# Optimization experiments

Hardware: AMD Instinct MI355X
Metric: run time of the kernel (lower is better)

The kernel has to match this reference:

```python
import jax, jax.numpy as jnp
import numpy as np
from jax import lax

# MinkowskiEngine semantics reproduced on a dense grid:
# - a sparse tensor's active set = voxels where any feature channel is nonzero
# - stride-1 conv: output coords == input coords  -> mask output with input mask
# - stride-2 conv (k=5, pad=2): output coords = unique(floor(c/2))  -> 2x2x2 max-pool of mask
# - GlobalPooling: mean of features over active output coords, per batch
# MinkowskiConvolution has no bias by default; MinkowskiLinear has one.

DN = ('NCDHW', 'OIDHW', 'NCDHW')

def conv3d(x, w, stride, pad):
    return lax.conv_general_dilated(
        x, w, (stride, stride, stride), [(pad, pad)] * 3, dimension_numbers=DN)

def pool_mask(m):
    # occupancy of stride-2 output coords: any active voxel in each 2x2x2 block
    B, T, H, W = m.shape
    return m.reshape(B, T // 2, 2, H // 2, 2, W // 2, 2).max(axis=(2, 4, 6))

def setup_inputs() -> dict:
    key = jax.random.key(0)
    ks = jax.random.split(key, 7)
    B, T, C, H, W = 16, 128, 2, 34, 34
    vals = jax.random.normal(ks[0], (B, T, C, H, W), jnp.float32)
    keep = jax.random.bernoulli(ks[1], 0.05, (B, T, 1, H, W)).astype(jnp.float32)
    x = vals * keep
    w1 = jax.random.normal(ks[2], (32, 2, 5, 5, 5), jnp.float32) * 0.05
    w2 = jax.random.normal(ks[3], (64, 32, 5, 5, 5), jnp.float32) * 0.05
    w3 = jax.random.normal(ks[4], (128, 64, 3, 3, 3), jnp.float32) * 0.05
    wl = jax.random.normal(ks[5], (10, 128), jnp.float32) * 0.05
    bl = jnp.zeros((10,), jnp.float32)
    return {"x": x, "w1": w1, "w2": w2, "w3": w3, "wl": wl, "bl": bl}

def reference(x, w1, w2, w3, wl, bl):
    # x: [B, T, C, H, W] -> permute(0,2,1,3,4) -> [B, C, T, H, W]
    dense = jnp.transpose(x, (0, 2, 1, 3, 4))
    # active coordinate set of ME.to_sparse(dense)
    mask = (jnp.abs(dense).sum(axis=1) > 0).astype(dense.dtype)  # [B, T, H, W]
    mask = lax.stop_gradient(mask)
    m1 = mask[:, None]
    h = conv3d(dense, w1, 1, 2) * m1                         # k5 s1, out coords = in coords
    mask2 = pool_mask(mask)                                  # stride-2 output occupancy
    m2 = mask2[:, None]
    h = jax.nn.relu(conv3d(h, w2, 2, 2)) * m2                # k5 s2 + ReLU
    h = jax.nn.relu(conv3d(h, w3, 1, 1)) * m2                # k3 s1 + ReLU
    cnt = jnp.maximum(mask2.sum(axis=(1, 2, 3)), 1.0)[:, None]
    pooled = h.sum(axis=(2, 3, 4)) / cnt                     # global avg over active coords -> [B,128]
    logits = pooled @ wl.T + bl                              # MinkowskiLinear(128,10)
    return jax.nn.softmax(jax.nn.relu(logits), axis=-1)      # ReLU -> Softmax -> ToFeature [B,10]
```

## Files before the change

kernel.cpp:

```cpp
#include <hip/hip_runtime.h>

#define BB 16
#define TT 128
#define HH 34
#define WW 34
#define HWSZ (HH*WW)
#define NP1 (BB*TT*HH*WW)
#define TD 64
#define HD 17
#define WD 17
#define NP2 (BB*TD*HD*WD)
#define NW1 (NP1/64)
#define NW2 (NP2/64)
#define CAP1 262144
#define CAP2 131072
#define G2 1024
#define G3 512

typedef __attribute__((ext_vector_type(8))) short bf16x8;
typedef __attribute__((ext_vector_type(4))) float f32x4;

__device__ inline unsigned short f2bf(float f) {
  unsigned u = __float_as_uint(f);
  unsigned r = (u + 0x7fff + ((u >> 16) & 1)) >> 16;
  return (unsigned short)r;
}
__device__ inline float bf2f(unsigned short s) {
  return __uint_as_float((unsigned)s << 16);
}

__global__ void k_ballot1(const float* __restrict__ x, unsigned long long* __restrict__ b1) {
  int i = blockIdx.x * 256 + threadIdx.x;
  int hw = i % HWSZ;
  int bt = i / HWSZ;
  const float* px = x + (size_t)bt * 2 * HWSZ + hw;
  bool act = (fabsf(px[0]) + fabsf(px[HWSZ])) > 0.0f;
  unsigned long long m = __ballot(act);
  if ((threadIdx.x & 63) == 0) b1[i >> 6] = m;
}

__global__ void k_ballot2(const unsigned long long* __restrict__ b1,
                          unsigned long long* __restrict__ b2) {
  int i = blockIdx.x * 256 + threadIdx.x;
  if (i >= NP2) return;
  int ow = i % WD; int r = i / WD;
  int oh = r % HD; r /= HD;
  int od = r % TD; int b = r / TD;
  bool act = false;
  for (int dt = 0; dt < 2; dt++)
    for (int dh = 0; dh < 2; dh++)
      for (int dw = 0; dw < 2; dw++) {
        int t = od * 2 + dt, h = oh * 2 + dh, w = ow * 2 + dw;
        int lin = ((b * TT + t) * HH + h) * WW + w;
        if ((b1[lin >> 6] >> (lin & 63)) & 1ull) act = true;
      }
  unsigned long long m = __ballot(act);
  if ((threadIdx.x & 63) == 0) b2[i >> 6] = m;
}

__global__ __launch_bounds__(1024) void k_scan(
    const unsigned long long* __restrict__ b1, const unsigned long long* __restrict__ b2,
    int* __restrict__ wb1, int* __restrict__ wb2,
    int* __restrict__ counter1, int* __restrict__ counter2, float* __restrict__ cnt) {
  __shared__ int wsum[16];
  __shared__ int wpre[16];
  __shared__ int tots[2];
  int tid = threadIdx.x, lane = tid & 63, wv = tid >> 6;

  const int CH1 = (NW1 + 1023) / 1024;
  int lo = tid * CH1, hi = min(lo + CH1, NW1);
  int s = 0;
  for (int i = lo; i < hi; i++) s += __popcll(b1[i]);
  int sc = s;
  #pragma unroll
  for (int d = 1; d < 64; d <<= 1) { int y = __shfl_up(sc, d); if (lane >= d) sc += y; }
  if (lane == 63) wsum[wv] = sc;
  __syncthreads();
  if (wv == 0 && lane < 16) {
    int v = wsum[lane];
    int p = v;
    #pragma unroll
    for (int d = 1; d < 16; d <<= 1) { int y = __shfl_up(p, d); if (lane >= d) p += y; }
    wpre[lane] = p - v;
    if (lane == 15) tots[0] = p;
  }
  __syncthreads();
  {
    int base = wpre[wv] + (sc - s);
    for (int i = lo; i < hi; i++) { wb1[i] = base; base += __popcll(b1[i]); }
  }
  if (tid == 0) *counter1 = tots[0];
  __syncthreads();

  const int CH2 = (NW2 + 1023) / 1024;
  lo = tid * CH2; hi = min(lo + CH2, NW2);
  s = 0;
  for (int i = lo; i < hi; i++) s += __popcll(b2[i]);
  sc = s;
  #pragma unroll
  for (int d = 1; d < 64; d <<= 1) { int y = __shfl_up(sc, d); if (lane >= d) sc += y; }
  if (lane == 63) wsum[wv] = sc;
  __syncthreads();
  if (wv == 0 && lane < 16) {
    int v = wsum[lane];
    int p = v;
    #pragma unroll
    for (int d = 1; d < 16; d <<= 1) { int y = __shfl_up(p, d); if (lane >= d) p += y; }
    wpre[lane] = p - v;
    if (lane == 15) tots[1] = p;
  }
  __syncthreads();
  {
    int base = wpre[wv] + (sc - s);
    for (int i = lo; i < hi; i++) { wb2[i] = base; base += __popcll(b2[i]); }
  }
  if (tid == 0) *counter2 = tots[1];
  __syncthreads();
  if (tid < 16) {
    int c0 = wb2[tid * 289];
    int c1 = (tid == 15) ? tots[1] : wb2[(tid + 1) * 289];
    cnt[tid] = (float)(c1 - c0);
  }
}

__global__ void k_fill1(const unsigned long long* __restrict__ b1,
                        const int* __restrict__ wb1, int* __restrict__ idx1) {
  int i = blockIdx.x * 256 + threadIdx.x;
  unsigned long long m = b1[i >> 6];
  int lane = i & 63;
  int p = -1;
  if ((m >> lane) & 1ull) {
    p = wb1[i >> 6] + __popcll(m & ((1ull << lane) - 1ull));
    if (p >= CAP1) p = -1;
  }
  idx1[i] = p;
}

__global__ void k_fill2(const unsigned long long* __restrict__ b2,
                        const int* __restrict__ wb2,
                        int* __restrict__ idx2, int* __restrict__ list2) {
  int i = blockIdx.x * 256 + threadIdx.x;
  if (i >= NP2) return;
  unsigned long long m = b2[i >> 6];
  int lane = i & 63;
  int p = -1;
  if ((m >> lane) & 1ull) {
    p = wb2[i >> 6] + __popcll(m & ((1ull << lane) - 1ull));
    if (p < CAP2) list2[p] = i; else p = -1;
  }
  idx2[i] = p;
}

__global__ __launch_bounds__(256) void k_conv1e(
    const float* __restrict__ x, const float* __restrict__ w1,
    const unsigned long long* __restrict__ b1, const int* __restrict__ wb1,
    unsigned short* __restrict__ h1c) {
  __shared__ unsigned short w1s[8000];
  __shared__ unsigned int plist[384];
  __shared__ unsigned long long q[4][128];
  __shared__ int pcnt;
  int tid = threadIdx.x;
  int b = blockIdx.x >> 7;
  int t0 = blockIdx.x & 127;
  if (tid == 0) pcnt = 0;
  for (int j = tid; j < 8000; j += 256) w1s[j] = f2bf(w1[j]);
  __syncthreads();
  int slabbase = (b * TT + t0) * HWSZ;
  for (int hw = tid; hw < HWSZ; hw += 256) {
    int lin = slabbase + hw;
    unsigned long long m = b1[lin >> 6];
    int ln = lin & 63;
    if ((m >> ln) & 1ull) {
      int p = wb1[lin >> 6] + __popcll(m & ((1ull << ln) - 1ull));
      if (p < CAP1) {
        int s = atomicAdd(&pcnt, 1);
        if (s < 384) plist[s] = ((unsigned)p << 11) | (unsigned)hw;
      }
    }
  }
  __syncthreads();
  int n = min(pcnt, 384);
  int lane = tid & 63, wid = tid >> 6;
  int oc = lane & 31, c = lane >> 5;
  int woff = (oc * 2 + c) * 125;
  int csh = c * 16;
  int kt = lane / 5, kh = lane - kt * 5;
  const float* xb = x + (size_t)b * TT * 2 * HWSZ;
  for (int li = wid; li < n; li += 4) {
    unsigned e = plist[li];
    int hw = e & 0x7ff;
    int p = e >> 11;
    int h_ = hw / 34, w_ = hw - h_ * 34;
    int cntA = 0;
    unsigned m5 = 0;
    int t2 = 0, h2 = 0;
    if (lane < 25) {
      t2 = t0 + kt - 2;
      h2 = h_ + kh - 2;
      if ((unsigned)t2 < TT && (unsigned)h2 < HH) {
        int kwmin = (w_ < 2) ? (2 - w_) : 0;
        int kwmax = (w_ > 31) ? (35 - w_) : 4;
        int lin = ((b * TT + t2) * HH + h2) * WW + (w_ + kwmin - 2);
        int wi = lin >> 6, sh = lin & 63;
        unsigned long long v = b1[wi] >> sh;
        if (sh > 59) v |= b1[wi + 1] << (64 - sh);
        m5 = ((unsigned)v & ((1u << (kwmax - kwmin + 1)) - 1u)) << kwmin;
        cntA = __popc(m5);
      }
    }
    int inc = cntA;
    #pragma unroll
    for (int d = 1; d < 64; d <<= 1) { int y = __shfl_up(inc, d); if (lane >= d) inc += y; }
    int off = inc - cntA;
    int ne = __shfl(inc, 63);
    unsigned mm = m5;
    while (mm) {
      int kw = __ffs(mm) - 1; mm &= mm - 1;
      int w2 = w_ + kw - 2;
      int xoff = (t2 * 2) * HWSZ + h2 * 34 + w2;
      unsigned short xv0 = f2bf(xb[xoff]);
      unsigned short xv1 = f2bf(xb[xoff + HWSZ]);
      int tap = (kt * 5 + kh) * 5 + kw;
      q[wid][off++] = (unsigned long long)((unsigned)xv0 | ((unsigned)xv1 << 16)) |
                      ((unsigned long long)tap << 32);
    }
    float acc = 0.f;
    for (int e2 = 0; e2 < ne; e2++) {
      unsigned long long ent = q[wid][e2];
      int tap = (int)(ent >> 32);
      float xv = bf2f((unsigned short)((ent >> csh) & 0xffffull));
      acc += xv * bf2f(w1s[woff + tap]);
    }
    float other = __shfl_down(acc, 32);
    if (lane < 32) h1c[(size_t)p * 32 + oc] = f2bf(acc + other);
  }
}

__global__ void k_tw2b(const float* __restrict__ w2, unsigned short* __restrict__ w2b) {
  int i = blockIdx.x * blockDim.x + threadIdx.x;
  if (i >= 125 * 64 * 32) return;
  int c = i & 31; int r = i >> 5;
  int oc = r & 63; int tap = r >> 6;
  w2b[i] = f2bf(w2[((size_t)oc * 32 + c) * 125 + tap]);
}
__global__ void k_tw3b(const float* __restrict__ w3, unsigned short* __restrict__ w3b) {
  int i = blockIdx.x * blockDim.x + threadIdx.x;
  if (i >= 27 * 128 * 64) return;
  int c = i & 63; int r = i >> 6;
  int oc = r & 127; int tap = r >> 7;
  w3b[i] = f2bf(w3[((size_t)oc * 64 + c) * 27 + tap]);
}

#define S2 40
#define M2 128
__global__ __launch_bounds__(256) void k_conv2m(
    const unsigned short* __restrict__ h1c,
    const unsigned short* __restrict__ w2b,
    const int* __restrict__ idx1,
    const int* __restrict__ list2, const int* __restrict__ counter2,
    unsigned short* __restrict__ h2c) {
  __shared__ __align__(16) unsigned short As[2][M2 * S2];
  __shared__ __align__(16) unsigned short Bs[2][64 * S2];
  __shared__ int4 mc[M2];
  __shared__ int klut[125];
  int tid = threadIdx.x;
  int lane = tid & 63, wid = tid >> 6;
  int fr = lane & 15, fq = lane >> 4;
  int wr = wid * 32;
  if (tid < 125) {
    int kt = tid / 25, r2 = tid - kt * 25;
    klut[tid] = kt | ((r2 / 5) << 4) | ((r2 % 5) << 8);
  }
  int count2 = min(*counter2, CAP2);
  int nchunk = (count2 + M2 - 1) >> 7;
  int aspos = tid >> 1, asq = tid & 1;
  int bspos = tid >> 2, bsq = tid & 3;
  int chid = (blockIdx.x & 7) * (G2 >> 3) + (blockIdx.x >> 3);
  __syncthreads();
  for (int ch = chid; ch < nchunk; ch += gridDim.x) {
    __syncthreads();
    if (tid < M2) {
      int p = ch * M2 + tid;
      int m = (p < count2) ? list2[p] : -1;
      int4 qq; qq.x = -1; qq.y = 0; qq.z = 0; qq.w = 0;
      if (m >= 0) {
        int ow = m % WD; int r = m / WD;
        int oh = r % HD; r /= HD;
        qq.x = r / TD; qq.y = r % TD; qq.z = oh; qq.w = ow;
      }
      mc[tid] = qq;
    }
    __syncthreads();
    int4 q = mc[aspos];
    int tb = q.y * 2 - 2, hb = q.z * 2 - 2, wbv = q.w * 2 - 2;
    bool bok = q.x >= 0;
    auto rowfor = [&](int tap) -> int {
      int k = klut[tap];
      int t = tb + (k & 15), h = hb + ((k >> 4) & 15), w = wbv + (k >> 8);
      int row = -1;
      if (bok && (unsigned)t < TT && (unsigned)h < HH && (unsigned)w < WW)
        row = idx1[((q.x * TT + t) * HH + h) * WW + w];
      return row;
    };
    f32x4 acc[2][4];
    #pragma unroll
    for (int i = 0; i < 2; i++)
      #pragma unroll
      for (int j = 0; j < 4; j++) acc[i][j] = (f32x4){0.f, 0.f, 0.f, 0.f};
    int rowN1;
    int4 rA0 = {0,0,0,0}, rA1 = {0,0,0,0}, rB;
    {
      int r0 = rowfor(0);
      if (r0 >= 0) {
        const unsigned short* s = h1c + (size_t)r0 * 32 + asq * 16;
        rA0 = *(const int4*)s;
        rA1 = *(const int4*)(s + 8);
      }
      rB = *(const int4*)(w2b + (size_t)bspos * 32 + bsq * 8);
      rowN1 = rowfor(1);
    }
    for (int tap = 0; tap < 125; ++tap) {
      int bsel = tap & 1;
      {
        unsigned short* ad = &As[bsel][aspos * S2 + asq * 16];
        *(int4*)(ad) = rA0;
        *(int4*)(ad + 8) = rA1;
        *(int4*)(&Bs[bsel][bspos * S2 + bsq * 8]) = rB;
      }
      bool more = tap < 124;
      if (more) {
        int4 v0 = {0,0,0,0}, v1 = {0,0,0,0};
        if (rowN1 >= 0) {
          const unsigned short* s = h1c + (size_t)rowN1 * 32 + asq * 16;
          v0 = *(const int4*)s;
          v1 = *(const int4*)(s + 8);
        }
        rA0 = v0; rA1 = v1;
        rB = *(const int4*)(w2b + (size_t)(tap + 1) * 2048 + bspos * 32 + bsq * 8);
        rowN1 = (tap < 123) ? rowfor(tap + 2) : -1;
      }
      __syncthreads();
      const unsigned short* ap = &As[bsel][(wr + fr) * S2 + fq * 8];
      const unsigned short* bp = &Bs[bsel][fr * S2 + fq * 8];
      bf16x8 a0 = *(const bf16x8*)ap;
      bf16x8 a1 = *(const bf16x8*)(ap + 16 * S2);
      #pragma unroll
      for (int ni = 0; ni < 4; ni++) {
        bf16x8 bfrag = *(const bf16x8*)(bp + ni * 16 * S2);
        acc[0][ni] = __builtin_amdgcn_mfma_f32_16x16x32_bf16(a0, bfrag, acc[0][ni], 0, 0, 0);
        acc[1][ni] = __builtin_amdgcn_mfma_f32_16x16x32_bf16(a1, bfrag, acc[1][ni], 0, 0, 0);
      }
    }
    int base = ch * M2;
    #pragma unroll
    for (int mi = 0; mi < 2; mi++)
      #pragma unroll
      for (int ni = 0; ni < 4; ni++)
        #pragma unroll
        for (int j = 0; j < 4; j++) {
          int r = wr + mi * 16 + fq * 4 + j;
          int p = base + r;
          if (p < count2) {
            int col = ni * 16 + fr;
            h2c[(size_t)p * 64 + col] = f2bf(fmaxf(acc[mi][ni][j], 0.f));
          }
        }
  }
}

#define S3 72
#define SH3 132
__global__ __launch_bounds__(256) void k_conv3m(
    const unsigned short* __restrict__ h2c,
    const unsigned short* __restrict__ w3b,
    const int* __restrict__ idx2,
    const int* __restrict__ list2, const int* __restrict__ counter2,
    float* __restrict__ partial) {
  __shared__ __align__(16) unsigned short As[2][64 * S3];
  __shared__ __align__(16) unsigned short Bs[2][128 * S3];
  __shared__ float pools[2048];
  __shared__ int rowsL[27 * 64];
  __shared__ int4 mc[64];
  __shared__ int posb[64];
  int tid = threadIdx.x;
  int lane = tid & 63, wid = tid >> 6;
  int fr = lane & 15, fq = lane >> 4;
  int wr = (wid >> 1) * 32, wc = (wid & 1) * 64;
  for (int j = tid; j < 2048; j += 256) pools[j] = 0.f;
  int count2 = min(*counter2, CAP2);
  int nchunk = (count2 + 63) >> 6;
  int spos = tid >> 2, sq = tid & 3;
  int boc = tid >> 1, bh = tid & 1;
  int chid = (blockIdx.x & 7) * (G3 >> 3) + (blockIdx.x >> 3);
  for (int ch = chid; ch < nchunk; ch += gridDim.x) {
    __syncthreads();
    if (tid < 64) {
      int p = ch * 64 + tid;
      int m = (p < count2) ? list2[p] : -1;
      int4 q; q.x = -1; q.y = 0; q.z = 0; q.w = 0;
      if (m >= 0) {
        int ow = m % WD; int r = m / WD;
        int oh = r % HD; r /= HD;
        q.x = r / TD; q.y = r % TD; q.z = oh; q.w = ow;
      }
      mc[tid] = q;
      posb[tid] = (q.x >= 0) ? q.x : 0;
    }
    __syncthreads();
    for (int j = tid; j < 27 * 64; j += 256) {
      int tap = j >> 6, pos = j & 63;
      int4 q = mc[pos];
      int row = -1;
      if (q.x >= 0) {
        int dt = tap / 9 - 1, dh = (tap / 3) % 3 - 1, dw = tap % 3 - 1;
        int t = q.y + dt, h = q.z + dh, w = q.w + dw;
        if ((unsigned)t < TD && (unsigned)h < HD && (unsigned)w < WD)
          row = idx2[((q.x * TD + t) * HD + h) * WD + w];
      }
      rowsL[j] = row;
    }
    __syncthreads();
    f32x4 acc[2][4];
    #pragma unroll
    for (int i = 0; i < 2; i++)
      #pragma unroll
      for (int j = 0; j < 4; j++) acc[i][j] = (f32x4){0.f, 0.f, 0.f, 0.f};
    int4 rA0 = {0, 0, 0, 0}, rA1 = {0, 0, 0, 0};
    {
      int row = rowsL[spos];
      if (row >= 0) {
        const unsigned short* s = h2c + (size_t)row * 64 + sq * 16;
        rA0 = *(const int4*)s;
        rA1 = *(const int4*)(s + 8);
      }
    }
    int4 rB0, rB1, rB2, rB3;
    {
      const unsigned short* wsrc = w3b + (size_t)boc * 64 + bh * 32;
      rB0 = *(const int4*)(wsrc);
      rB1 = *(const int4*)(wsrc + 8);
      rB2 = *(const int4*)(wsrc + 16);
      rB3 = *(const int4*)(wsrc + 24);
    }
    for (int tap = 0; tap < 27; tap++) {
      int bsel = tap & 1;
      {
        unsigned short* ad = &As[bsel][spos * S3 + sq * 16];
        *(int4*)(ad) = rA0;
        *(int4*)(ad + 8) = rA1;
        unsigned short* bd = &Bs[bsel][boc * S3 + bh * 32];
        *(int4*)(bd) = rB0;
        *(int4*)(bd + 8) = rB1;
        *(int4*)(bd + 16) = rB2;
        *(int4*)(bd + 24) = rB3;
      }
      if (tap < 26) {
        int row = rowsL[(tap + 1) * 64 + spos];
        int4 v0 = {0, 0, 0, 0}, v1 = {0, 0, 0, 0};
        if (row >= 0) {
          const unsigned short* s = h2c + (size_t)row * 64 + sq * 16;
          v0 = *(const int4*)s;
          v1 = *(const int4*)(s + 8);
        }
        rA0 = v0; rA1 = v1;
        const unsigned short* wsrc = w3b + ((size_t)(tap + 1) * 128 + boc) * 64 + bh * 32;
        rB0 = *(const int4*)(wsrc);
        rB1 = *(const int4*)(wsrc + 8);
        rB2 = *(const int4*)(wsrc + 16);
        rB3 = *(const int4*)(wsrc + 24);
      }
      __syncthreads();
      const unsigned short* ap = &As[bsel][(wr + fr) * S3 + fq * 8];
      const unsigned short* bp = &Bs[bsel][(wc + fr) * S3 + fq * 8];
      #pragma unroll
      for (int kk = 0; kk < 2; kk++) {
        bf16x8 a0 = *(const bf16x8*)(ap + kk * 32);
        bf16x8 a1 = *(const bf16x8*)(ap + 16 * S3 + kk * 32);
        #pragma unroll
        for (int ni = 0; ni < 4; ni++) {
          bf16x8 bfrag = *(const bf16x8*)(bp + ni * 16 * S3 + kk * 32);
          acc[0][ni] = __builtin_amdgcn_mfma_f32_16x16x32_bf16(a0, bfrag, acc[0][ni], 0, 0, 0);
          acc[1][ni] = __builtin_amdgcn_mfma_f32_16x16x32_bf16(a1, bfrag, acc[1][ni], 0, 0, 0);
        }
      }
    }
    __syncthreads();
    unsigned short* h3 = &As[0][0];
    #pragma unroll
    for (int mi = 0; mi < 2; mi++)
      #pragma unroll
      for (int ni = 0; ni < 4; ni++)
        #pragma unroll
        for (int j = 0; j < 4; j++) {
          int r = wr + mi * 16 + fq * 4 + j;
          int col = wc + ni * 16 + fr;
          h3[r * SH3 + col] = f2bf(fmaxf(acc[mi][ni][j], 0.f));
        }
    __syncthreads();
    if (tid < 128) {
      for (int r = 0; r < 64; r++)
        pools[posb[r] * 128 + tid] += bf2f(h3[r * SH3 + tid]);
    }
  }
  __syncthreads();
  for (int j = tid; j < 2048; j += 256)
    partial[(size_t)blockIdx.x * 2048 + j] = pools[j];
}

__global__ __launch_bounds__(256) void k_red(
    const float* __restrict__ partial, float* __restrict__ pooled) {
  __shared__ float red[256];
  int o = blockIdx.x * 16 + (threadIdx.x & 15);
  int sl = threadIdx.x >> 4;
  float s = 0.f;
  for (int g = sl; g < G3; g += 16) s += partial[(size_t)g * 2048 + o];
  red[threadIdx.x] = s;
  __syncthreads();
  if (threadIdx.x < 16) {
    float t = 0.f;
    #pragma unroll
    for (int k = 0; k < 16; k++) t += red[k * 16 + threadIdx.x];
    pooled[o] = t;
  }
}

__global__ void k_fin(const float* __restrict__ pooled, const float* __restrict__ cnt,
                      const float* __restrict__ wl, const float* __restrict__ bl,
                      float* __restrict__ out) {
  __shared__ float pr[128];
  __shared__ float lg[10];
  int b = blockIdx.x;
  int tid = threadIdx.x;
  pr[tid] = pooled[b * 128 + tid] / fmaxf(cnt[b], 1.0f);
  __syncthreads();
  if (tid < 10) {
    float acc = bl[tid];
    for (int j = 0; j < 128; j++) acc += pr[j] * wl[tid * 128 + j];
    lg[tid] = fmaxf(acc, 0.f);
  }
  __syncthreads();
  if (tid == 0) {
    float mx = lg[0];
    for (int k = 1; k < 10; k++) mx = fmaxf(mx, lg[k]);
    float se = 0.f;
    for (int k = 0; k < 10; k++) se += expf(lg[k] - mx);
    for (int k = 0; k < 10; k++) out[b * 10 + k] = expf(lg[k] - mx) / se;
  }
}

extern "C" void kernel_launch(void* const* d_in, const int* in_sizes, int n_in,
                              void* d_out, int out_size, void* d_ws, size_t ws_size,
                              hipStream_t stream) {
  const float* x  = (const float*)d_in[0];
  const float* w1 = (const float*)d_in[1];
  const float* w2 = (const float*)d_in[2];
  const float* w3 = (const float*)d_in[3];
  const float* wl = (const float*)d_in[4];
  const float* bl = (const float*)d_in[5];
  float* out = (float*)d_out;

  float* ws = (float*)d_ws;
  int* counter1 = (int*)(ws + 0);
  int* counter2 = (int*)(ws + 1);
  float* cnt = ws + 16;
  float* pooled = ws + 32;
  size_t off = 2080;
  unsigned long long* b1 = (unsigned long long*)(ws + off); off += NW1 * 2 + 2;
  unsigned long long* b2 = (unsigned long long*)(ws + off); off += NW2 * 2;
  int* wb1 = (int*)(ws + off); off += NW1;
  int* wb2 = (int*)(ws + off); off += NW2;
  int* idx1 = (int*)(ws + off); off += NP1;
  unsigned short* h1c = (unsigned short*)(ws + off); off += (size_t)CAP1 * 16;
  int* idx2 = (int*)(ws + off); off += NP2;
  int* list2 = (int*)(ws + off); off += CAP2;
  unsigned short* h2c = (unsigned short*)(ws + off); off += (size_t)CAP2 * 32;
  unsigned short* w2b = (unsigned short*)(ws + off); off += 128000;
  unsigned short* w3b = (unsigned short*)(ws + off); off += 110592;
  float* partial = ws + off; off += (size_t)G3 * 2048;

  hipMemsetAsync(d_ws, 0, 256, stream);

  k_tw2b<<<(256000 + 255) / 256, 256, 0, stream>>>(w2, w2b);
  k_tw3b<<<(221184 + 255) / 256, 256, 0, stream>>>(w3, w3b);
  k_ballot1<<<NP1 / 256, 256, 0, stream>>>(x, b1);
  k_ballot2<<<(NP2 + 255) / 256, 256, 0, stream>>>(b1, b2);
  k_scan<<<1, 1024, 0, stream>>>(b1, b2, wb1, wb2, counter1, counter2, cnt);
  k_conv1e<<<2048, 256, 0, stream>>>(x, w1, b1, wb1, h1c);
  k_fill1<<<NP1 / 256, 256, 0, stream>>>(b1, wb1, idx1);
  k_fill2<<<(NP2 + 255) / 256, 256, 0, stream>>>(b2, wb2, idx2, list2);
  k_conv2m<<<G2, 256, 0, stream>>>(h1c, w2b, idx1, list2, counter2, h2c);
  k_conv3m<<<G3, 256, 0, stream>>>(h2c, w3b, idx2, list2, counter2, partial);
  k_red<<<128, 256, 0, stream>>>(partial, pooled);
  k_fin<<<16, 128, 0, stream>>>(pooled, cnt, wl, bl, out);
}
```

Measured before the change: 376.8 us.

## Load conv2 MFMA fragments directly from global memory, dropping LDS staging

```diff
diff --git a/kernel.cpp b/kernel.cpp
--- a/kernel.cpp
+++ b/kernel.cpp
@@ -251,7 +251,6 @@
   w3b[i] = f2bf(w3[((size_t)oc * 64 + c) * 27 + tap]);
 }
 
-#define S2 40
 #define M2 128
 __global__ __launch_bounds__(256) void k_conv2m(
     const unsigned short* __restrict__ h1c,
@@ -259,8 +258,6 @@
     const int* __restrict__ idx1,
     const int* __restrict__ list2, const int* __restrict__ counter2,
     unsigned short* __restrict__ h2c) {
-  __shared__ __align__(16) unsigned short As[2][M2 * S2];
-  __shared__ __align__(16) unsigned short Bs[2][64 * S2];
   __shared__ int4 mc[M2];
   __shared__ int klut[125];
   int tid = threadIdx.x;
@@ -273,9 +270,8 @@
   }
   int count2 = min(*counter2, CAP2);
   int nchunk = (count2 + M2 - 1) >> 7;
-  int aspos = tid >> 1, asq = tid & 1;
-  int bspos = tid >> 2, bsq = tid & 3;
   int chid = (blockIdx.x & 7) * (G2 >> 3) + (blockIdx.x >> 3);
+  const bf16x8 z = {0,0,0,0,0,0,0,0};
   __syncthreads();
   for (int ch = chid; ch < nchunk; ch += gridDim.x) {
     __syncthreads();
@@ -291,15 +287,25 @@
       mc[tid] = qq;
     }
     __syncthreads();
-    int4 q = mc[aspos];
-    int tb = q.y * 2 - 2, hb = q.z * 2 - 2, wbv = q.w * 2 - 2;
-    bool bok = q.x >= 0;
-    auto rowfor = [&](int tap) -> int {
+    int4 q0 = mc[wr + fr];
+    int4 q1 = mc[wr + 16 + fr];
+    int tb0 = q0.y * 2 - 2, hb0 = q0.z * 2 - 2, wb0 = q0.w * 2 - 2;
+    int tb1 = q1.y * 2 - 2, hb1 = q1.z * 2 - 2, wb1v = q1.w * 2 - 2;
+    bool ok0 = q0.x >= 0, ok1 = q1.x >= 0;
+    auto rowfor0 = [&](int tap) -> int {
       int k = klut[tap];
-      int t = tb + (k & 15), h = hb + ((k >> 4) & 15), w = wbv + (k >> 8);
+      int t = tb0 + (k & 15), h = hb0 + ((k >> 4) & 15), w = wb0 + (k >> 8);
       int row = -1;
-      if (bok && (unsigned)t < TT && (unsigned)h < HH && (unsigned)w < WW)
-        row = idx1[((q.x * TT + t) * HH + h) * WW + w];
+      if (ok0 && (unsigned)t < TT && (unsigned)h < HH && (unsigned)w < WW)
+        row = idx1[((q0.x * TT + t) * HH + h) * WW + w];
+      return row;
+    };
+    auto rowfor1 = [&](int tap) -> int {
+      int k = klut[tap];
+      int t = tb1 + (k & 15), h = hb1 + ((k >> 4) & 15), w = wb1v + (k >> 8);
+      int row = -1;
+      if (ok1 && (unsigned)t < TT && (unsigned)h < HH && (unsigned)w < WW)
+        row = idx1[((q1.x * TT + t) * HH + h) * WW + w];
       return row;
     };
     f32x4 acc[2][4];
@@ -307,48 +313,36 @@
     for (int i = 0; i < 2; i++)
       #pragma unroll
       for (int j = 0; j < 4; j++) acc[i][j] = (f32x4){0.f, 0.f, 0.f, 0.f};
-    int rowN1;
-    int4 rA0 = {0,0,0,0}, rA1 = {0,0,0,0}, rB;
-    {
-      int r0 = rowfor(0);
-      if (r0 >= 0) {
-        const unsigned short* s = h1c + (size_t)r0 * 32 + asq * 16;
-        rA0 = *(const int4*)s;
-        rA1 = *(const int4*)(s + 8);
-      }
-      rB = *(const int4*)(w2b + (size_t)bspos * 32 + bsq * 8);
-      rowN1 = rowfor(1);
-    }
+    const unsigned short* wB = w2b + (size_t)fr * 32 + fq * 8;
+    int r0 = rowfor0(0), r1 = rowfor1(0);
+    bf16x8 a0 = (r0 >= 0) ? *(const bf16x8*)(h1c + (size_t)r0 * 32 + fq * 8) : z;
+    bf16x8 a1 = (r1 >= 0) ? *(const bf16x8*)(h1c + (size_t)r1 * 32 + fq * 8) : z;
+    bf16x8 bfr[4];
+    #pragma unroll
+    for (int ni = 0; ni < 4; ni++) bfr[ni] = *(const bf16x8*)(wB + ni * 512);
+    int rn0 = rowfor0(1), rn1 = rowfor1(1);
     for (int tap = 0; tap < 125; ++tap) {
-      int bsel = tap & 1;
-      {
-        unsigned short* ad = &As[bsel][aspos * S2 + asq * 16];
-        *(int4*)(ad) = rA0;
-        *(int4*)(ad + 8) = rA1;
-        *(int4*)(&Bs[bsel][bspos * S2 + bsq * 8]) = rB;
-      }
       bool more = tap < 124;
+      bf16x8 na0 = z, na1 = z, nb[4];
+      int rw0 = -1, rw1 = -1;
       if (more) {
-        int4 v0 = {0,0,0,0}, v1 = {0,0,0,0};
-        if (rowN1 >= 0) {
-          const unsigned short* s = h1c + (size_t)rowN1 * 32 + asq * 16;
-          v0 = *(const int4*)s;
-          v1 = *(const int4*)(s + 8);
-        }
-        rA0 = v0; rA1 = v1;
-        rB = *(const int4*)(w2b + (size_t)(tap + 1) * 2048 + bspos * 32 + bsq * 8);
-        rowN1 = (tap < 123) ? rowfor(tap + 2) : -1;
-      }
-      __syncthreads();
-      const unsigned short* ap = &As[bsel][(wr + fr) * S2 + fq * 8];
-      const unsigned short* bp = &Bs[bsel][fr * S2 + fq * 8];
-      bf16x8 a0 = *(const bf16x8*)ap;
-      bf16x8 a1 = *(const bf16x8*)(ap + 16 * S2);
+        if (rn0 >= 0) na0 = *(const bf16x8*)(h1c + (size_t)rn0 * 32 + fq * 8);
+        if (rn1 >= 0) na1 = *(const bf16x8*)(h1c + (size_t)rn1 * 32 + fq * 8);
+        const unsigned short* wt = wB + (size_t)(tap + 1) * 2048;
+        #pragma unroll
+        for (int ni = 0; ni < 4; ni++) nb[ni] = *(const bf16x8*)(wt + ni * 512);
+        if (tap < 123) { rw0 = rowfor0(tap + 2); rw1 = rowfor1(tap + 2); }
+      }
       #pragma unroll
       for (int ni = 0; ni < 4; ni++) {
-        bf16x8 bfrag = *(const bf16x8*)(bp + ni * 16 * S2);
-        acc[0][ni] = __builtin_amdgcn_mfma_f32_16x16x32_bf16(a0, bfrag, acc[0][ni], 0, 0, 0);
-        acc[1][ni] = __builtin_amdgcn_mfma_f32_16x16x32_bf16(a1, bfrag, acc[1][ni], 0, 0, 0);
+        acc[0][ni] = __builtin_amdgcn_mfma_f32_16x16x32_bf16(a0, bfr[ni], acc[0][ni], 0, 0, 0);
+        acc[1][ni] = __builtin_amdgcn_mfma_f32_16x16x32_bf16(a1, bfr[ni], acc[1][ni], 0, 0, 0);
+      }
+      if (more) {
+        a0 = na0; a1 = na1;
+        #pragma unroll
+        for (int ni = 0; ni < 4; ni++) bfr[ni] = nb[ni];
+        rn0 = rw0; rn1 = rw1;
       }
     }
     int base = ch * M2;
```

Result: slower. 514.7 us (+36.6%).

## Deepen register prefetch to three taps in conv2/conv3 and relax barrier waits

Applied to the files above, without the earlier changes.

```diff
diff --git a/kernel.cpp b/kernel.cpp
--- a/kernel.cpp
+++ b/kernel.cpp
@@ -307,50 +307,65 @@
     for (int i = 0; i < 2; i++)
       #pragma unroll
       for (int j = 0; j < 4; j++) acc[i][j] = (f32x4){0.f, 0.f, 0.f, 0.f};
-    int rowN1;
-    int4 rA0 = {0,0,0,0}, rA1 = {0,0,0,0}, rB;
+    int4 A0_0 = {0,0,0,0}, A1_0 = {0,0,0,0}, B_0;
+    int4 A0_1 = {0,0,0,0}, A1_1 = {0,0,0,0}, B_1;
+    int4 A0_2 = {0,0,0,0}, A1_2 = {0,0,0,0}, B_2;
     {
-      int r0 = rowfor(0);
-      if (r0 >= 0) {
-        const unsigned short* s = h1c + (size_t)r0 * 32 + asq * 16;
-        rA0 = *(const int4*)s;
-        rA1 = *(const int4*)(s + 8);
-      }
-      rB = *(const int4*)(w2b + (size_t)bspos * 32 + bsq * 8);
-      rowN1 = rowfor(1);
-    }
-    for (int tap = 0; tap < 125; ++tap) {
-      int bsel = tap & 1;
-      {
-        unsigned short* ad = &As[bsel][aspos * S2 + asq * 16];
-        *(int4*)(ad) = rA0;
-        *(int4*)(ad + 8) = rA1;
-        *(int4*)(&Bs[bsel][bspos * S2 + bsq * 8]) = rB;
-      }
-      bool more = tap < 124;
-      if (more) {
-        int4 v0 = {0,0,0,0}, v1 = {0,0,0,0};
-        if (rowN1 >= 0) {
-          const unsigned short* s = h1c + (size_t)rowN1 * 32 + asq * 16;
-          v0 = *(const int4*)s;
-          v1 = *(const int4*)(s + 8);
-        }
-        rA0 = v0; rA1 = v1;
-        rB = *(const int4*)(w2b + (size_t)(tap + 1) * 2048 + bspos * 32 + bsq * 8);
-        rowN1 = (tap < 123) ? rowfor(tap + 2) : -1;
-      }
-      __syncthreads();
-      const unsigned short* ap = &As[bsel][(wr + fr) * S2 + fq * 8];
-      const unsigned short* bp = &Bs[bsel][fr * S2 + fq * 8];
-      bf16x8 a0 = *(const bf16x8*)ap;
-      bf16x8 a1 = *(const bf16x8*)(ap + 16 * S2);
-      #pragma unroll
-      for (int ni = 0; ni < 4; ni++) {
-        bf16x8 bfrag = *(const bf16x8*)(bp + ni * 16 * S2);
-        acc[0][ni] = __builtin_amdgcn_mfma_f32_16x16x32_bf16(a0, bfrag, acc[0][ni], 0, 0, 0);
-        acc[1][ni] = __builtin_amdgcn_mfma_f32_16x16x32_bf16(a1, bfrag, acc[1][ni], 0, 0, 0);
-      }
-    }
+      int r = rowfor(0);
+      if (r >= 0) { const unsigned short* s_ = h1c + (size_t)r * 32 + asq * 16;
+        A0_0 = *(const int4*)s_; A1_0 = *(const int4*)(s_ + 8); }
+      B_0 = *(const int4*)(w2b + (size_t)bspos * 32 + bsq * 8);
+    }
+    {
+      int r = rowfor(1);
+      if (r >= 0) { const unsigned short* s_ = h1c + (size_t)r * 32 + asq * 16;
+        A0_1 = *(const int4*)s_; A1_1 = *(const int4*)(s_ + 8); }
+      B_1 = *(const int4*)(w2b + (size_t)2048 + bspos * 32 + bsq * 8);
+    }
+    {
+      int r = rowfor(2);
+      if (r >= 0) { const unsigned short* s_ = h1c + (size_t)r * 32 + asq * 16;
+        A0_2 = *(const int4*)s_; A1_2 = *(const int4*)(s_ + 8); }
+      B_2 = *(const int4*)(w2b + (size_t)2 * 2048 + bspos * 32 + bsq * 8);
+    }
+#define C2_TAP(T, A0r, A1r, Br) {                                          \
+      int bsel = (T) & 1;                                                   \
+      unsigned short* ad = &As[bsel][aspos * S2 + asq * 16];                \
+      *(int4*)(ad) = A0r;                                                   \
+      *(int4*)(ad + 8) = A1r;                                               \
+      *(int4*)(&Bs[bsel][bspos * S2 + bsq * 8]) = Br;                       \
+      if ((T) + 3 < 126) {                                                  \
+        int r_ = ((T) + 3 <= 124) ? rowfor((T) + 3) : -1;                   \
+        A0r = make_int4(0,0,0,0); A1r = make_int4(0,0,0,0);                 \
+        if (r_ >= 0) { const unsigned short* s_ = h1c + (size_t)r_ * 32 + asq * 16; \
+          A0r = *(const int4*)s_; A1r = *(const int4*)(s_ + 8); }           \
+        Br = *(const int4*)(w2b + (size_t)min((T) + 3, 124) * 2048 + bspos * 32 + bsq * 8); \
+      }                                                                     \
+      asm volatile("s_waitcnt lgkmcnt(0)" ::: "memory");                    \
+      __builtin_amdgcn_s_barrier();                                         \
+      const unsigned short* ap = &As[bsel][(wr + fr) * S2 + fq * 8];        \
+      const unsigned short* bp = &Bs[bsel][fr * S2 + fq * 8];               \
+      bf16x8 a0 = *(const bf16x8*)ap;                                       \
+      bf16x8 a1 = *(const bf16x8*)(ap + 16 * S2);                           \
+      bf16x8 bf0 = *(const bf16x8*)(bp);                                    \
+      bf16x8 bf1 = *(const bf16x8*)(bp + 16 * S2);                          \
+      bf16x8 bf2v = *(const bf16x8*)(bp + 32 * S2);                         \
+      bf16x8 bf3 = *(const bf16x8*)(bp + 48 * S2);                          \
+      acc[0][0] = __builtin_amdgcn_mfma_f32_16x16x32_bf16(a0, bf0, acc[0][0], 0, 0, 0); \
+      acc[1][0] = __builtin_amdgcn_mfma_f32_16x16x32_bf16(a1, bf0, acc[1][0], 0, 0, 0); \
+      acc[0][1] = __builtin_amdgcn_mfma_f32_16x16x32_bf16(a0, bf1, acc[0][1], 0, 0, 0); \
+      acc[1][1] = __builtin_amdgcn_mfma_f32_16x16x32_bf16(a1, bf1, acc[1][1], 0, 0, 0); \
+      acc[0][2] = __builtin_amdgcn_mfma_f32_16x16x32_bf16(a0, bf2v, acc[0][2], 0, 0, 0); \
+      acc[1][2] = __builtin_amdgcn_mfma_f32_16x16x32_bf16(a1, bf2v, acc[1][2], 0, 0, 0); \
+      acc[0][3] = __builtin_amdgcn_mfma_f32_16x16x32_bf16(a0, bf3, acc[0][3], 0, 0, 0); \
+      acc[1][3] = __builtin_amdgcn_mfma_f32_16x16x32_bf16(a1, bf3, acc[1][3], 0, 0, 0); \
+    }
+    for (int tbase = 0; tbase < 126; tbase += 3) {
+      C2_TAP(tbase + 0, A0_0, A1_0, B_0);
+      C2_TAP(tbase + 1, A0_1, A1_1, B_1);
+      C2_TAP(tbase + 2, A0_2, A1_2, B_2);
+    }
+#undef C2_TAP
     int base = ch * M2;
     #pragma unroll
     for (int mi = 0; mi < 2; mi++)
@@ -425,65 +440,72 @@
     for (int i = 0; i < 2; i++)
       #pragma unroll
       for (int j = 0; j < 4; j++) acc[i][j] = (f32x4){0.f, 0.f, 0.f, 0.f};
-    int4 rA0 = {0, 0, 0, 0}, rA1 = {0, 0, 0, 0};
+    int4 A0_0 = {0,0,0,0}, A1_0 = {0,0,0,0}, B0_0, B1_0, B2_0, B3_0;
+    int4 A0_1 = {0,0,0,0}, A1_1 = {0,0,0,0}, B0_1, B1_1, B2_1, B3_1;
+    int4 A0_2 = {0,0,0,0}, A1_2 = {0,0,0,0}, B0_2, B1_2, B2_2, B3_2;
     {
-      int row = rowsL[spos];
-      if (row >= 0) {
-        const unsigned short* s = h2c + (size_t)row * 64 + sq * 16;
-        rA0 = *(const int4*)s;
-        rA1 = *(const int4*)(s + 8);
-      }
-    }
-    int4 rB0, rB1, rB2, rB3;
+      int r = rowsL[spos];
+      if (r >= 0) { const unsigned short* s_ = h2c + (size_t)r * 64 + sq * 16;
+        A0_0 = *(const int4*)s_; A1_0 = *(const int4*)(s_ + 8); }
+      const unsigned short* ws_ = w3b + (size_t)boc * 64 + bh * 32;
+      B0_0 = *(const int4*)(ws_); B1_0 = *(const int4*)(ws_ + 8);
+      B2_0 = *(const int4*)(ws_ + 16); B3_0 = *(const int4*)(ws_ + 24);
+    }
     {
-      const unsigned short* wsrc = w3b + (size_t)boc * 64 + bh * 32;
-      rB0 = *(const int4*)(wsrc);
-      rB1 = *(const int4*)(wsrc + 8);
-      rB2 = *(const int4*)(wsrc + 16);
-      rB3 = *(const int4*)(wsrc + 24);
-    }
-    for (int tap = 0; tap < 27; tap++) {
-      int bsel = tap & 1;
-      {
-        unsigned short* ad = &As[bsel][spos * S3 + sq * 16];
-        *(int4*)(ad) = rA0;
-        *(int4*)(ad + 8) = rA1;
-        unsigned short* bd = &Bs[bsel][boc * S3 + bh * 32];
-        *(int4*)(bd) = rB0;
-        *(int4*)(bd + 8) = rB1;
-        *(int4*)(bd + 16) = rB2;
-        *(int4*)(bd + 24) = rB3;
-      }
-      if (tap < 26) {
-        int row = rowsL[(tap + 1) * 64 + spos];
-        int4 v0 = {0, 0, 0, 0}, v1 = {0, 0, 0, 0};
-        if (row >= 0) {
-          const unsigned short* s = h2c + (size_t)row * 64 + sq * 16;
-          v0 = *(const int4*)s;
-          v1 = *(const int4*)(s + 8);
-        }
-        rA0 = v0; rA1 = v1;
-        const unsigned short* wsrc = w3b + ((size_t)(tap + 1) * 128 + boc) * 64 + bh * 32;
-        rB0 = *(const int4*)(wsrc);
-        rB1 = *(const int4*)(wsrc + 8);
-        rB2 = *(const int4*)(wsrc + 16);
-        rB3 = *(const int4*)(wsrc + 24);
-      }
-      __syncthreads();
-      const unsigned short* ap = &As[bsel][(wr + fr) * S3 + fq * 8];
-      const unsigned short* bp = &Bs[bsel][(wc + fr) * S3 + fq * 8];
-      #pragma unroll
-      for (int kk = 0; kk < 2; kk++) {
-        bf16x8 a0 = *(const bf16x8*)(ap + kk * 32);
-        bf16x8 a1 = *(const bf16x8*)(ap + 16 * S3 + kk * 32);
-        #pragma unroll
-        for (int ni = 0; ni < 4; ni++) {
-          bf16x8 bfrag = *(const bf16x8*)(bp + ni * 16 * S3 + kk * 32);
-          acc[0][ni] = __builtin_amdgcn_mfma_f32_16x16x32_bf16(a0, bfrag, acc[0][ni], 0, 0, 0);
-          acc[1][ni] = __builtin_amdgcn_mfma_f32_16x16x32_bf16(a1, bfrag, acc[1][ni], 0, 0, 0);
-        }
-      }
-    }
+      int r = rowsL[64 + spos];
+      if (r >= 0) { const unsigned short* s_ = h2c + (size_t)r * 64 + sq * 16;
+        A0_1 = *(const int4*)s_; A1_1 = *(const int4*)(s_ + 8); }
+      const unsigned short* ws_ = w3b + ((size_t)128 + boc) * 64 + bh * 32;
+      B0_1 = *(const int4*)(ws_); B1_1 = *(const int4*)(ws_ + 8);
+      B2_1 = *(const int4*)(ws_ + 16); B3_1 = *(const int4*)(ws_ + 24);
+    }
+    {
+      int r = rowsL[128 + spos];
+      if (r >= 0) { const unsigned short* s_ = h2c + (size_t)r * 64 + sq * 16;
+        A0_2 = *(const int4*)s_; A1_2 = *(const int4*)(s_ + 8); }
+      const unsigned short* ws_ = w3b + ((size_t)256 + boc) * 64 + bh * 32;
+      B0_2 = *(const int4*)(ws_); B1_2 = *(const int4*)(ws_ + 8);
+      B2_2 = *(const int4*)(ws_ + 16); B3_2 = *(const int4*)(ws_ + 24);
+    }
+#define C3_TAP(T, A0r, A1r, B0r, B1r, B2r, B3r) {                          \
+      int bsel = (T) & 1;                                                   \
+      unsigned short* ad = &As[bsel][spos * S3 + sq * 16];                  \
+      *(int4*)(ad) = A0r;                                                   \
+      *(int4*)(ad + 8) = A1r;                                               \
+      unsigned short* bd = &Bs[bsel][boc * S3 + bh * 32];                   \
+      *(int4*)(bd) = B0r; *(int4*)(bd + 8) = B1r;                           \
+      *(int4*)(bd + 16) = B2r; *(int4*)(bd + 24) = B3r;                     \
+      if ((T) + 3 <= 26) {                                                  \
+        int r_ = rowsL[((T) + 3) * 64 + spos];                              \
+        A0r = make_int4(0,0,0,0); A1r = make_int4(0,0,0,0);                 \
+        if (r_ >= 0) { const unsigned short* s_ = h2c + (size_t)r_ * 64 + sq * 16; \
+          A0r = *(const int4*)s_; A1r = *(const int4*)(s_ + 8); }           \
+        const unsigned short* ws_ = w3b + ((size_t)((T) + 3) * 128 + boc) * 64 + bh * 32; \
+        B0r = *(const int4*)(ws_); B1r = *(const int4*)(ws_ + 8);           \
+        B2r = *(const int4*)(ws_ + 16); B3r = *(const int4*)(ws_ + 24);     \
+      }                                                                     \
+      asm volatile("s_waitcnt lgkmcnt(0)" ::: "memory");                    \
+      __builtin_amdgcn_s_barrier();                                         \
+      const unsigned short* ap = &As[bsel][(wr + fr) * S3 + fq * 8];        \
+      const unsigned short* bp = &Bs[bsel][(wc + fr) * S3 + fq * 8];        \
+      _Pragma("unroll")                                                     \
+      for (int kk = 0; kk < 2; kk++) {                                      \
+        bf16x8 a0 = *(const bf16x8*)(ap + kk * 32);                         \
+        bf16x8 a1 = *(const bf16x8*)(ap + 16 * S3 + kk * 32);               \
+        _Pragma("unroll")                                                   \
+        for (int ni = 0; ni < 4; ni++) {                                    \
+          bf16x8 bfrag = *(const bf16x8*)(bp + ni * 16 * S3 + kk * 32);     \
+          acc[0][ni] = __builtin_amdgcn_mfma_f32_16x16x32_bf16(a0, bfrag, acc[0][ni], 0, 0, 0); \
+          acc[1][ni] = __builtin_amdgcn_mfma_f32_16x16x32_bf16(a1, bfrag, acc[1][ni], 0, 0, 0); \
+        }                                                                   \
+      }                                                                     \
+    }
+    for (int tbase = 0; tbase < 27; tbase += 3) {
+      C3_TAP(tbase + 0, A0_0, A1_0, B0_0, B1_0, B2_0, B3_0);
+      C3_TAP(tbase + 1, A0_1, A1_1, B0_1, B1_1, B2_1, B3_1);
+      C3_TAP(tbase + 2, A0_2, A1_2, B0_2, B1_2, B2_2, B3_2);
+    }
+#undef C3_TAP
     __syncthreads();
     unsigned short* h3 = &As[0][0];
     #pragma unroll
```

Measured after the change: 462.3 us. 1.23x slower.
